# Performance work log

Hardware: AMD Instinct MI355X
Metric: run time of the kernel (lower is better)

The kernel has to match this reference:

```python
import jax, jax.numpy as jnp
import numpy as np

B, S, E, P = 4, 2048, 1024, 4096

def setup_inputs() -> dict:
    key = jax.random.key(0)
    kx, kk, kv = jax.random.split(key, 3)
    x = jax.random.normal(kx, (B, S, E), dtype=jnp.float32)
    K = jax.random.normal(kk, (P, E), dtype=jnp.float32)
    V = jax.random.normal(kv, (P, E), dtype=jnp.float32)
    return {"x": x, "K": K, "V": V}

def reference(x, K, V):
    # scores: [B, S, P] = x @ K^T scaled by 1/sqrt(E)
    scale = jnp.asarray(x.shape[-1], x.dtype) ** -0.5
    scores = jnp.einsum('bse,pe->bsp', x, K) * scale
    attn = jax.nn.softmax(scores, axis=-1)
    # output: [B, S, E] = attn @ V
    return jnp.einsum('bsp,pe->bse', attn, V)
```

## Files before the change

kernel.cpp:

```cpp
#include <hip/hip_runtime.h>
#include <hip/hip_bf16.h>

typedef __attribute__((ext_vector_type(8))) short bf16x8;
typedef __attribute__((ext_vector_type(4))) float f32x4;
typedef __attribute__((ext_vector_type(8))) unsigned short u16x8;

__device__ __forceinline__ unsigned short f2bf(float f) {
  union { float f; unsigned u; } c; c.f = f;
  unsigned u = c.u;
  u = (u + 0x7FFFu + ((u >> 16) & 1u)) >> 16;
  return (unsigned short)u;
}

__device__ __forceinline__ void gld_lds16(const void* g, void* l) {
  __builtin_amdgcn_global_load_lds(
      (__attribute__((address_space(1))) unsigned int*)g,
      (__attribute__((address_space(3))) unsigned int*)l,
      16, 0, 0);
}

#define BAR() asm volatile("s_barrier" ::: "memory")

__global__ void cvt_all(const float* __restrict__ x, unsigned short* __restrict__ x16,
                        const float* __restrict__ Kw, unsigned short* __restrict__ K16,
                        const float* __restrict__ V, unsigned short* __restrict__ Vt,
                        float* __restrict__ lsum) {
  const int b = blockIdx.x;
  const int tid = threadIdx.x;
  if (b < 32) lsum[b * 256 + tid] = 0.f;

  if (b < 6144) {
    const float* in;
    unsigned short* out;
    int i;
    if (b < 4096) {
      in = x; out = x16; i = (b * 256 + tid) * 8;
    } else {
      in = Kw; out = K16; i = ((b - 4096) * 256 + tid) * 8;
    }
    const float4* p = (const float4*)(in + i);
    float4 a = p[0], bb = p[1];
    u16x8 r;
    r[0] = f2bf(a.x); r[1] = f2bf(a.y); r[2] = f2bf(a.z); r[3] = f2bf(a.w);
    r[4] = f2bf(bb.x); r[5] = f2bf(bb.y); r[6] = f2bf(bb.z); r[7] = f2bf(bb.w);
    *(u16x8*)(out + i) = r;
  } else {
    __shared__ unsigned short t[64][65];
    const int tile = b - 6144;
    const int p0 = (tile & 63) * 64;
    const int e0 = (tile >> 6) * 64;
    const int tx = tid & 63;
    const int ty = tid >> 6;
#pragma unroll
    for (int i = 0; i < 16; ++i) {
      int p = ty + i * 4;
      t[p][tx] = f2bf(V[(size_t)(p0 + p) * 1024 + e0 + tx]);
    }
    __syncthreads();
    const int op = (tid & 7) * 8;
    const int oe = tid >> 3;
#pragma unroll
    for (int h = 0; h < 2; ++h) {
      int e = oe + h * 32;
      u16x8 r;
#pragma unroll
      for (int i = 0; i < 8; ++i) r[i] = t[op + i][e];
      *(u16x8*)(Vt + (size_t)(e0 + e) * 4096 + p0 + op) = r;
    }
  }
}

template <int EPI>
__global__ __launch_bounds__(512, 2) void gemm8p(
    const unsigned short* __restrict__ A, const unsigned short* __restrict__ B,
    unsigned short* __restrict__ Pout, float* __restrict__ lsum,
    float* __restrict__ Cout, const float* __restrict__ lin, float scale) {
  constexpr int BM = EPI ? 128 : 256;
  constexpr int Kd = EPI ? 4096 : 1024;
  constexpr int Nc = EPI ? 1024 : 4096;
  constexpr int NT = Kd / 64;
  constexpr int AU = BM / 128;
  constexpr int NU = AU + 2;
  constexpr int M_rep = BM / 32;
  constexpr int PH = M_rep / 2;

  __shared__ __align__(16) char lds[2 * NU * 16384];

  const int tid = threadIdx.x;
  const int lane = tid & 63;
  const int w = tid >> 6;
  const int wm = w >> 2;
  const int wn = w & 3;
  const int q = lane >> 4;
  const int ml = lane & 15;

  const int bid = blockIdx.x;
  const int wg = (bid & 7) * (EPI ? 32 : 64) + (bid >> 3);
  const int m_t = EPI ? (wg >> 2) : (wg >> 4);
  const int n_t = EPI ? (wg & 3) : (wg & 15);
  const int row0 = m_t * BM;
  const int col0 = n_t * 256;

  const int cr = tid >> 3;
  const int ss = (tid & 7) ^ (cr & 7);
  char* ldsw = lds + w * 1024;

  const int ccB = (q ^ (ml & 7)) * 16;
  const int aOff = (EPI ? 0 : wm) * 16384 + ((EPI ? wm * 64 : 0) + ml) * 128 + ccB;
  const int bOff = (AU + (wn >> 1)) * 16384 + ((wn & 1) * 64 + ml) * 128 + ccB;

  f32x4 acc[M_rep][4] = {};

  auto stA = [&](int a, int t, int buf) {
    const unsigned short* s = A + (size_t)(row0 + a * 128 + cr) * Kd + t * 64 + ss * 8;
    char* d = ldsw + (buf * NU + a) * 16384;
    gld_lds16(s, d);
    gld_lds16(s + (size_t)64 * Kd, d + 8192);
  };
  auto stB = [&](int b, int t, int buf) {
    const unsigned short* s = B + (size_t)(col0 + b * 128 + cr) * Kd + t * 64 + ss * 8;
    char* d = ldsw + (buf * NU + AU + b) * 16384;
    gld_lds16(s, d);
    gld_lds16(s + (size_t)64 * Kd, d + 8192);
  };

#pragma unroll
  for (int a = 0; a < AU; ++a) stA(a, 0, 0);
  stB(0, 0, 0); stB(1, 0, 0);
  stB(0, 1, 1); stB(1, 1, 1);
  asm volatile("s_waitcnt vmcnt(4)" ::: "memory");
  BAR();

  for (int g = 0; g < NT; ++g) {
    const char* base = lds + (g & 1) * (NU * 16384);
    const int tA = (g + 1) & (NT - 1);
    const int bufA = (g + 1) & 1;
    const int tB = (g + 2) & (NT - 1);
    const int bufB = g & 1;

    bf16x8 bF[4][2];
#pragma unroll
    for (int ni = 0; ni < 4; ++ni)
#pragma unroll
      for (int ks = 0; ks < 2; ++ks)
        bF[ni][ks] = *(const bf16x8*)(base + (bOff ^ (ks * 64)) + ni * 2048);

#pragma unroll
    for (int p = 0; p < PH; ++p) {
      bf16x8 aF[2][2];
#pragma unroll
      for (int i = 0; i < 2; ++i)
#pragma unroll
        for (int ks = 0; ks < 2; ++ks)
          aF[i][ks] = *(const bf16x8*)(base + ((aOff ^ (ks * 64)) + (2 * p + i) * 2048));

      if constexpr (EPI == 0) {
        if (p == 0) stA(0, tA, bufA);
        else if (p == 1) stA(1, tA, bufA);
        else if (p == 2) stB(0, tB, bufB);
        else stB(1, tB, bufB);
      } else {
        if (p == 0) stA(0, tA, bufA);
        else { stB(0, tB, bufB); stB(1, tB, bufB); }
      }

      BAR();
      __builtin_amdgcn_s_setprio(1);
#pragma unroll
      for (int ks = 0; ks < 2; ++ks)
#pragma unroll
        for (int i = 0; i < 2; ++i)
#pragma unroll
          for (int ni = 0; ni < 4; ++ni)
            acc[2 * p + i][ni] = __builtin_amdgcn_mfma_f32_16x16x32_bf16(
                aF[i][ks], bF[ni][ks], acc[2 * p + i][ni], 0, 0, 0);
      __builtin_amdgcn_s_setprio(0);
      if (p == PH - 1) asm volatile("s_waitcnt vmcnt(4)" ::: "memory");
      BAR();
    }
  }

  if constexpr (EPI == 0) {
#pragma unroll
    for (int mi = 0; mi < M_rep; ++mi) {
#pragma unroll
      for (int j = 0; j < 4; ++j) {
        const int gr = row0 + wm * (BM / 2) + mi * 16 + q * 4 + j;
        float rsum = 0.f;
#pragma unroll
        for (int ni = 0; ni < 4; ++ni) {
          const int gc = col0 + wn * 64 + ni * 16 + ml;
          float pv = exp2f(acc[mi][ni][j] * scale);
          rsum += pv;
          Pout[(size_t)gr * Nc + gc] = f2bf(pv);
        }
        rsum += __shfl_xor(rsum, 1);
        rsum += __shfl_xor(rsum, 2);
        rsum += __shfl_xor(rsum, 4);
        rsum += __shfl_xor(rsum, 8);
        if (ml == 0) atomicAdd(&lsum[gr], rsum);
      }
    }
  } else {
#pragma unroll
    for (int mi = 0; mi < M_rep; ++mi) {
#pragma unroll
      for (int j = 0; j < 4; ++j) {
        const int gr = row0 + wm * (BM / 2) + mi * 16 + q * 4 + j;
        const float rl = 1.0f / lin[gr];
#pragma unroll
        for (int ni = 0; ni < 4; ++ni) {
          const int gc = col0 + wn * 64 + ni * 16 + ml;
          Cout[(size_t)gr * Nc + gc] = acc[mi][ni][j] * rl;
        }
      }
    }
  }
}

extern "C" void kernel_launch(void* const* d_in, const int* in_sizes, int n_in,
                              void* d_out, int out_size, void* d_ws,
                              size_t ws_size, hipStream_t stream) {
  const float* x = (const float*)d_in[0];
  const float* Kw = (const float*)d_in[1];
  const float* Vw = (const float*)d_in[2];
  float* out = (float*)d_out;
  char* ws = (char*)d_ws;

  unsigned short* x16  = (unsigned short*)(ws);
  unsigned short* K16  = (unsigned short*)(ws + (16u << 20));
  unsigned short* V16t = (unsigned short*)(ws + (24u << 20));
  float*          lsum = (float*)(ws + (32u << 20));
  unsigned short* P16  = (unsigned short*)(ws + (33u << 20));

  cvt_all<<<7168, 256, 0, stream>>>(x, x16, Kw, K16, Vw, V16t, lsum);

  gemm8p<0><<<512, 512, 0, stream>>>(
      x16, K16, P16, lsum, nullptr, nullptr,
      0.03125f * 1.44269504088896340736f);
  gemm8p<1><<<256, 512, 0, stream>>>(
      P16, V16t, nullptr, nullptr, out, lsum, 0.f);
}
```

Baseline: 257.3 us.

## Switch GEMMs to 128x128 tiles with 4-wave blocks and two-phase double buffering

Both GEMM kernels drop from 512-thread blocks with 256x256 or 128x256 tiles to 256-thread blocks with 128x128 tiles, which gives more workgroups (2048 and 512). Each K step is split into two MFMA phases, with the A and B prefetch loads interleaved between them. Barriers now wait on LDS counters before syncing. The smaller tiles trade less operand reuse per block and more global traffic for better occupancy and load balance across CUs.

```diff
diff --git a/kernel.cpp b/kernel.cpp
--- a/kernel.cpp
+++ b/kernel.cpp
@@ -19,7 +19,11 @@
       16, 0, 0);
 }
 
-#define BAR() asm volatile("s_barrier" ::: "memory")
+#define BARD()                                          \
+  do {                                                  \
+    asm volatile("s_waitcnt lgkmcnt(0)" ::: "memory");  \
+    asm volatile("s_barrier" ::: "memory");             \
+  } while (0)
 
 __global__ void cvt_all(const float* __restrict__ x, unsigned short* __restrict__ x16,
                         const float* __restrict__ Kw, unsigned short* __restrict__ K16,
@@ -71,121 +75,122 @@
 }
 
 template <int EPI>
-__global__ __launch_bounds__(512, 2) void gemm8p(
+__global__ __launch_bounds__(256, 2) void gemm_db(
     const unsigned short* __restrict__ A, const unsigned short* __restrict__ B,
     unsigned short* __restrict__ Pout, float* __restrict__ lsum,
     float* __restrict__ Cout, const float* __restrict__ lin, float scale) {
-  constexpr int BM = EPI ? 128 : 256;
   constexpr int Kd = EPI ? 4096 : 1024;
   constexpr int Nc = EPI ? 1024 : 4096;
   constexpr int NT = Kd / 64;
-  constexpr int AU = BM / 128;
-  constexpr int NU = AU + 2;
-  constexpr int M_rep = BM / 32;
-  constexpr int PH = M_rep / 2;
-
-  __shared__ __align__(16) char lds[2 * NU * 16384];
+
+  __shared__ __align__(16) char lds[65536];
 
   const int tid = threadIdx.x;
   const int lane = tid & 63;
   const int w = tid >> 6;
-  const int wm = w >> 2;
-  const int wn = w & 3;
+  const int wm = w >> 1;
+  const int wn = w & 1;
   const int q = lane >> 4;
   const int ml = lane & 15;
 
   const int bid = blockIdx.x;
-  const int wg = (bid & 7) * (EPI ? 32 : 64) + (bid >> 3);
-  const int m_t = EPI ? (wg >> 2) : (wg >> 4);
-  const int n_t = EPI ? (wg & 3) : (wg & 15);
-  const int row0 = m_t * BM;
-  const int col0 = n_t * 256;
+  const int wg = (bid & 7) * (EPI ? 64 : 256) + (bid >> 3);
+  const int m_t = EPI ? (wg >> 3) : (wg >> 5);
+  const int n_t = EPI ? (wg & 7) : (wg & 31);
+  const int row0 = m_t * 128;
+  const int col0 = n_t * 128;
 
   const int cr = tid >> 3;
   const int ss = (tid & 7) ^ (cr & 7);
+  const unsigned short* pA = A + (size_t)(row0 + cr) * Kd + ss * 8;
+  const unsigned short* pB = B + (size_t)(col0 + cr) * Kd + ss * 8;
   char* ldsw = lds + w * 1024;
 
-  const int ccB = (q ^ (ml & 7)) * 16;
-  const int aOff = (EPI ? 0 : wm) * 16384 + ((EPI ? wm * 64 : 0) + ml) * 128 + ccB;
-  const int bOff = (AU + (wn >> 1)) * 16384 + ((wn & 1) * 64 + ml) * 128 + ccB;
-
-  f32x4 acc[M_rep][4] = {};
-
-  auto stA = [&](int a, int t, int buf) {
-    const unsigned short* s = A + (size_t)(row0 + a * 128 + cr) * Kd + t * 64 + ss * 8;
-    char* d = ldsw + (buf * NU + a) * 16384;
-    gld_lds16(s, d);
-    gld_lds16(s + (size_t)64 * Kd, d + 8192);
+  const int cc0 = (q ^ (ml & 7)) * 16;
+  const int aOff = (wm * 64 + ml) * 128 + cc0;
+  const int bOff = 16384 + (wn * 64 + ml) * 128 + cc0;
+
+  f32x4 acc[4][4] = {};
+
+  auto stA = [&](int t, int buf) {
+    const unsigned short* s = pA + t * 64;
+    char* d = ldsw + buf * 32768;
+#pragma unroll
+    for (int j = 0; j < 4; ++j) gld_lds16(s + (size_t)j * 32 * Kd, d + j * 4096);
   };
-  auto stB = [&](int b, int t, int buf) {
-    const unsigned short* s = B + (size_t)(col0 + b * 128 + cr) * Kd + t * 64 + ss * 8;
-    char* d = ldsw + (buf * NU + AU + b) * 16384;
-    gld_lds16(s, d);
-    gld_lds16(s + (size_t)64 * Kd, d + 8192);
+  auto stB = [&](int t, int buf) {
+    const unsigned short* s = pB + t * 64;
+    char* d = ldsw + buf * 32768 + 16384;
+#pragma unroll
+    for (int j = 0; j < 4; ++j) gld_lds16(s + (size_t)j * 32 * Kd, d + j * 4096);
   };
 
-#pragma unroll
-  for (int a = 0; a < AU; ++a) stA(a, 0, 0);
-  stB(0, 0, 0); stB(1, 0, 0);
-  stB(0, 1, 1); stB(1, 1, 1);
+  stA(0, 0); stB(0, 0);
+  stB(1 & (NT - 1), 1);
   asm volatile("s_waitcnt vmcnt(4)" ::: "memory");
-  BAR();
-
+  __builtin_amdgcn_s_barrier();
+
+#pragma unroll 2
   for (int g = 0; g < NT; ++g) {
-    const char* base = lds + (g & 1) * (NU * 16384);
+    const char* base = lds + (g & 1) * 32768;
     const int tA = (g + 1) & (NT - 1);
-    const int bufA = (g + 1) & 1;
     const int tB = (g + 2) & (NT - 1);
-    const int bufB = g & 1;
-
-    bf16x8 bF[4][2];
+
+    bf16x8 bF[4][2], a0[2][2];
 #pragma unroll
     for (int ni = 0; ni < 4; ++ni)
 #pragma unroll
       for (int ks = 0; ks < 2; ++ks)
-        bF[ni][ks] = *(const bf16x8*)(base + (bOff ^ (ks * 64)) + ni * 2048);
-
-#pragma unroll
-    for (int p = 0; p < PH; ++p) {
-      bf16x8 aF[2][2];
+        bF[ni][ks] = *(const bf16x8*)(base + ((bOff + ni * 2048) ^ (ks * 64)));
+#pragma unroll
+    for (int i = 0; i < 2; ++i)
+#pragma unroll
+      for (int ks = 0; ks < 2; ++ks)
+        a0[i][ks] = *(const bf16x8*)(base + ((aOff + i * 2048) ^ (ks * 64)));
+
+    stA(tA, (g + 1) & 1);
+
+    __builtin_amdgcn_s_setprio(1);
+#pragma unroll
+    for (int ks = 0; ks < 2; ++ks)
 #pragma unroll
       for (int i = 0; i < 2; ++i)
 #pragma unroll
-        for (int ks = 0; ks < 2; ++ks)
-          aF[i][ks] = *(const bf16x8*)(base + ((aOff ^ (ks * 64)) + (2 * p + i) * 2048));
-
-      if constexpr (EPI == 0) {
-        if (p == 0) stA(0, tA, bufA);
-        else if (p == 1) stA(1, tA, bufA);
-        else if (p == 2) stB(0, tB, bufB);
-        else stB(1, tB, bufB);
-      } else {
-        if (p == 0) stA(0, tA, bufA);
-        else { stB(0, tB, bufB); stB(1, tB, bufB); }
-      }
-
-      BAR();
-      __builtin_amdgcn_s_setprio(1);
+        for (int ni = 0; ni < 4; ++ni)
+          acc[i][ni] = __builtin_amdgcn_mfma_f32_16x16x32_bf16(
+              a0[i][ks], bF[ni][ks], acc[i][ni], 0, 0, 0);
+    __builtin_amdgcn_s_setprio(0);
+    BARD();
+
+    bf16x8 a1[2][2];
+#pragma unroll
+    for (int i = 0; i < 2; ++i)
 #pragma unroll
       for (int ks = 0; ks < 2; ++ks)
-#pragma unroll
-        for (int i = 0; i < 2; ++i)
-#pragma unroll
-          for (int ni = 0; ni < 4; ++ni)
-            acc[2 * p + i][ni] = __builtin_amdgcn_mfma_f32_16x16x32_bf16(
-                aF[i][ks], bF[ni][ks], acc[2 * p + i][ni], 0, 0, 0);
-      __builtin_amdgcn_s_setprio(0);
-      if (p == PH - 1) asm volatile("s_waitcnt vmcnt(4)" ::: "memory");
-      BAR();
-    }
+        a1[i][ks] = *(const bf16x8*)(base + ((aOff + (2 + i) * 2048) ^ (ks * 64)));
+
+    stB(tB, g & 1);
+
+    __builtin_amdgcn_s_setprio(1);
+#pragma unroll
+    for (int ks = 0; ks < 2; ++ks)
+#pragma unroll
+      for (int i = 0; i < 2; ++i)
+#pragma unroll
+        for (int ni = 0; ni < 4; ++ni)
+          acc[2 + i][ni] = __builtin_amdgcn_mfma_f32_16x16x32_bf16(
+              a1[i][ks], bF[ni][ks], acc[2 + i][ni], 0, 0, 0);
+    __builtin_amdgcn_s_setprio(0);
+    asm volatile("s_waitcnt vmcnt(4)" ::: "memory");
+    BARD();
   }
 
   if constexpr (EPI == 0) {
 #pragma unroll
-    for (int mi = 0; mi < M_rep; ++mi) {
+    for (int mi = 0; mi < 4; ++mi) {
 #pragma unroll
       for (int j = 0; j < 4; ++j) {
-        const int gr = row0 + wm * (BM / 2) + mi * 16 + q * 4 + j;
+        const int gr = row0 + wm * 64 + mi * 16 + q * 4 + j;
         float rsum = 0.f;
 #pragma unroll
         for (int ni = 0; ni < 4; ++ni) {
@@ -203,10 +208,10 @@
     }
   } else {
 #pragma unroll
-    for (int mi = 0; mi < M_rep; ++mi) {
+    for (int mi = 0; mi < 4; ++mi) {
 #pragma unroll
       for (int j = 0; j < 4; ++j) {
-        const int gr = row0 + wm * (BM / 2) + mi * 16 + q * 4 + j;
+        const int gr = row0 + wm * 64 + mi * 16 + q * 4 + j;
         const float rl = 1.0f / lin[gr];
 #pragma unroll
         for (int ni = 0; ni < 4; ++ni) {
@@ -235,9 +240,9 @@
 
   cvt_all<<<7168, 256, 0, stream>>>(x, x16, Kw, K16, Vw, V16t, lsum);
 
-  gemm8p<0><<<512, 512, 0, stream>>>(
+  gemm_db<0><<<2048, 256, 0, stream>>>(
       x16, K16, P16, lsum, nullptr, nullptr,
       0.03125f * 1.44269504088896340736f);
-  gemm8p<1><<<256, 512, 0, stream>>>(
+  gemm_db<1><<<512, 256, 0, stream>>>(
       P16, V16t, nullptr, nullptr, out, lsum, 0.f);
 }
```

Result: slower. 277.7 us (+8.0%).
